# Performance work log

Measured on AMD Instinct MI355X. Metric: run time of the kernel, lower is better.

Reference implementation:

```python
import jax, jax.numpy as jnp
import numpy as np

N_Q = 16
N_K = 16
D_QK = 64
D_V = 64
# torch module default scale=1.0 saturates softmax at feature width 1024;
# we use the conventional sqrt(d) scale for well-conditioned numerics.
SCALE = 32.0  # sqrt(N_Q * D_QK)
DROPOUT_P = 0.0  # dropout is identity at p=0


def setup_inputs() -> dict:
    key = jax.random.key(0)
    kq, kk, kv = jax.random.split(key, 3)
    S = 8192
    return {
        "query": jax.random.normal(kq, (S, N_Q, D_QK), dtype=jnp.float32),
        "key": jax.random.normal(kk, (S, N_K, D_QK), dtype=jnp.float32),
        "value": jax.random.normal(kv, (S, N_K, D_V), dtype=jnp.float32),
    }


def reference(query, key, value):
    # Flatten trailing (head, dim) into one feature axis, as the torch view does.
    q = query.reshape(-1, N_Q * D_QK)            # [S_q, 1024]
    k = key.reshape(-1, N_K * D_QK)              # [S_k, 1024]
    v = value.reshape(-1, N_K * D_V)             # [S_k, 1024]
    scores = jnp.matmul(q, k.T) / SCALE          # [S_q, S_k]
    attn = jax.nn.softmax(scores, axis=-1)       # dropout_p=0 -> identity
    out = jnp.matmul(attn, v)                    # [S_q, 1024]
    return out.reshape(query.shape[:-1] + (-1,))  # [S_q, N_Q, D_V]
```

## Files before the change

kernel.cpp:

```cpp
#include <hip/hip_runtime.h>
#include <hip/hip_bf16.h>


typedef __bf16 bf16x8 __attribute__((ext_vector_type(8)));
typedef float f32x4 __attribute__((ext_vector_type(4)));
typedef const __attribute__((address_space(1))) unsigned int* as1p;
typedef __attribute__((address_space(3))) unsigned int* as3p;
typedef unsigned short u16;

__device__ __forceinline__ u16 f2bf(float x) {
  unsigned u = __float_as_uint(x);
  u += 0x7fffu + ((u >> 16) & 1u);
  return (u16)(u >> 16);
}
__device__ __forceinline__ float bf2f(u16 b) { return __uint_as_float(((unsigned)b) << 16); }
__device__ __forceinline__ unsigned pack2(float lo, float hi) {
  return (unsigned)f2bf(lo) | ((unsigned)f2bf(hi) << 16);
}

#define BAR()   do { __builtin_amdgcn_s_barrier(); asm volatile("" ::: "memory"); } while (0)
#define VM(n)   do { asm volatile("s_waitcnt vmcnt(" #n ")" ::: "memory"); __builtin_amdgcn_sched_barrier(0); } while (0)

__global__ __launch_bounds__(256) void cvt_bf16(const float* __restrict__ in,
                                                unsigned short* __restrict__ out) {
  const size_t i = (size_t)blockIdx.x * 256 + threadIdx.x;
  const float4* p = (const float4*)in + i * 2;
  float4 a = p[0], b = p[1];
  uint4 o;
  o.x = pack2(a.x, a.y);
  o.y = pack2(a.z, a.w);
  o.z = pack2(b.x, b.y);
  o.w = pack2(b.z, b.w);
  ((uint4*)out)[i] = o;
}

__global__ __launch_bounds__(256) void transpose_bf16(const float* __restrict__ V,
                                                      unsigned short* __restrict__ VT) {
  __shared__ float t[64][65];
  const int rb = blockIdx.x * 64;
  const int cb = blockIdx.y * 64;
  const int tid = threadIdx.x;
#pragma unroll
  for (int it = 0; it < 4; ++it) {
    int r = it * 16 + (tid >> 4);
    int c = (tid & 15) * 4;
    float4 x = *(const float4*)(V + (size_t)(rb + r) * 1024 + cb + c);
    t[r][c] = x.x; t[r][c + 1] = x.y; t[r][c + 2] = x.z; t[r][c + 3] = x.w;
  }
  __syncthreads();
  const int j = tid & 63;
  const int c0 = (tid >> 6) * 16;
#pragma unroll
  for (int i = 0; i < 16; ++i) {
    int c = c0 + i;
    VT[(size_t)(cb + c) * 8192 + rb + j] = f2bf(t[j][c]);
  }
}

template <int BM, int DEPTH, int OUTMODE, int DEC>
__global__ __launch_bounds__(512, 2) void gemm_pl(const u16* __restrict__ A,
                                                  const u16* __restrict__ B,
                                                  void* __restrict__ Cv,
                                                  const float* __restrict__ inv,
                                                  float* __restrict__ partials,
                                                  int K, int ldc, float scale) {
  constexpr int MF = BM / 32;
  constexpr int MH = MF / 2;
  constexpr int LAJ = BM / 64;
  constexpr int LPT = LAJ + 4;
  constexpr int ABUF = BM * 128;
  constexpr int BBUF = 32768;
  constexpr int BUFSZ = ABUF + BBUF;
  __shared__ __align__(1024) char smem[DEPTH * BUFSZ];

  const int tid = threadIdx.x;
  const int lane = tid & 63, wave = tid >> 6;
  const int wr = wave >> 2, wc = wave & 3;
  const int lan15 = lane & 15, g = lane >> 4, l7 = lane & 7;

  const int nwg = gridDim.x;
  const int wg = (blockIdx.x & 7) * (nwg >> 3) + (blockIdx.x >> 3);
  int bm0, bn0;
  if constexpr (DEC == 0) {
    const int r = wg & 255;
    bm0 = (r >> 3) * 256;
    bn0 = (((wg >> 8) << 3) | (r & 7)) * 256;
  } else {
    const int chunk = wg >> 5;
    const int within = wg & 31;
    bm0 = (chunk * 8 + (within >> 2)) * BM;
    bn0 = (within & 3) * 256;
  }

  const int sr = tid >> 3;
  const int scb = ((tid & 7) ^ (sr & 7)) * 8;
  const u16* Ags = A + (size_t)(bm0 + sr) * K + scb;
  const u16* Bgs = B + (size_t)(bn0 + sr) * K + scb;

  const int sa0 = ((0 + g) ^ l7) * 16;
  const int sa1 = ((4 + g) ^ l7) * 16;
  const int abase = (wr * (BM / 2) + lan15) * 128;
  const int bbase = ABUF + (wc * 64 + lan15) * 128;

  f32x4 acc[MF][4];
#pragma unroll
  for (int m = 0; m < MF; ++m)
#pragma unroll
    for (int n = 0; n < 4; ++n) acc[m][n] = f32x4{0.f, 0.f, 0.f, 0.f};

  const int nt = K >> 6;

  auto ISSUE = [&](int t) {
    char* bb = smem + (t % DEPTH) * BUFSZ;
    const size_t ko = (size_t)t * 64;
#pragma unroll
    for (int j = 0; j < LAJ; ++j)
      __builtin_amdgcn_global_load_lds((as1p)(Ags + (size_t)j * 64 * K + ko),
                                       (as3p)(bb + j * 8192 + tid * 16), 16, 0, 0);
#pragma unroll
    for (int j = 0; j < 4; ++j)
      __builtin_amdgcn_global_load_lds((as1p)(Bgs + (size_t)j * 64 * K + ko),
                                       (as3p)(bb + ABUF + j * 8192 + tid * 16), 16, 0, 0);
  };

  bf16x8 A0[MH][2], A1[MH][2], B0[2][2], B1[2][2];

  auto RD_A0 = [&](int t) {
    const char* bp = smem + (t % DEPTH) * BUFSZ;
#pragma unroll
    for (int m = 0; m < MH; ++m) {
      A0[m][0] = *(const bf16x8*)(bp + abase + m * 2048 + sa0);
      A0[m][1] = *(const bf16x8*)(bp + abase + m * 2048 + sa1);
    }
  };
  auto RD_A1 = [&](int t) {
    const char* bp = smem + (t % DEPTH) * BUFSZ;
#pragma unroll
    for (int m = 0; m < MH; ++m) {
      A1[m][0] = *(const bf16x8*)(bp + abase + (MH + m) * 2048 + sa0);
      A1[m][1] = *(const bf16x8*)(bp + abase + (MH + m) * 2048 + sa1);
    }
  };
  auto RD_B0 = [&](int t) {
    const char* bp = smem + (t % DEPTH) * BUFSZ;
#pragma unroll
    for (int n = 0; n < 2; ++n) {
      B0[n][0] = *(const bf16x8*)(bp + bbase + n * 2048 + sa0);
      B0[n][1] = *(const bf16x8*)(bp + bbase + n * 2048 + sa1);
    }
  };
  auto RD_B1 = [&](int t) {
    const char* bp = smem + (t % DEPTH) * BUFSZ;
#pragma unroll
    for (int n = 0; n < 2; ++n) {
      B1[n][0] = *(const bf16x8*)(bp + bbase + (2 + n) * 2048 + sa0);
      B1[n][1] = *(const bf16x8*)(bp + bbase + (2 + n) * 2048 + sa1);
    }
  };

  auto Q = [&](bf16x8 (&a)[MH][2], bf16x8 (&b)[2][2], int mo, int no) {
    __builtin_amdgcn_s_setprio(1);
#pragma unroll
    for (int m = 0; m < MH; ++m)
#pragma unroll
      for (int n = 0; n < 2; ++n)
#pragma unroll
        for (int ks = 0; ks < 2; ++ks)
          acc[mo + m][no + n] = __builtin_amdgcn_mfma_f32_16x16x32_bf16(
              a[m][ks], b[n][ks], acc[mo + m][no + n], 0, 0, 0);
    __builtin_amdgcn_s_setprio(0);
  };

  ISSUE(0);
  if constexpr (DEPTH == 3) {
    ISSUE(1);
    if constexpr (LPT == 8) { VM(8); } else { VM(6); }
  } else {
    VM(0);
  }
  BAR();
  RD_A0(0); RD_B0(0);

  for (int t = 0; t < nt; ++t) {
    BAR();
    if constexpr (DEPTH == 2) {
      if (t + 1 < nt) ISSUE(t + 1);
    } else {
      if (t + 2 < nt) ISSUE(t + 2);
    }
    RD_B1(t);
    Q(A0, B0, 0, 0);
    RD_A1(t);
    Q(A0, B1, 0, 2);
    if constexpr (DEPTH == 2) {
      if (t + 1 < nt) { VM(0); }
    } else {
      if (t + 2 < nt) {
        if constexpr (LPT == 8) { VM(8); } else { VM(6); }
      } else if (t + 1 < nt) {
        VM(0);
      }
    }
    Q(A1, B0, MH, 0);
    if (t + 1 < nt) { RD_A0(t + 1); RD_B0(t + 1); }
    Q(A1, B1, MH, 2);
  }

  const int c0 = bn0 + wc * 64 + lan15;
  if constexpr (OUTMODE == 0) {
    u16* C = (u16*)Cv;
    const int cb4 = (bn0 >> 8) * 4 + wc;
#pragma unroll
    for (int m = 0; m < MF; ++m)
#pragma unroll
      for (int r = 0; r < 4; ++r) {
        const int row = bm0 + wr * (BM / 2) + m * 16 + g * 4 + r;
        float part = 0.f;
#pragma unroll
        for (int n = 0; n < 4; ++n) {
          float v = __expf(acc[m][n][r] * scale);
          C[(size_t)row * ldc + c0 + n * 16] = f2bf(v);
          part += v;
        }
        part += __shfl_xor(part, 1, 64);
        part += __shfl_xor(part, 2, 64);
        part += __shfl_xor(part, 4, 64);
        part += __shfl_xor(part, 8, 64);
        if (lan15 == 0) partials[(size_t)row * 128 + cb4] = part;
      }
  } else {
    float* C = (float*)Cv;
#pragma unroll
    for (int m = 0; m < MF; ++m)
#pragma unroll
      for (int r = 0; r < 4; ++r) {
        const int row = bm0 + wr * (BM / 2) + m * 16 + g * 4 + r;
        const float iv = inv ? inv[row] : 1.0f;
#pragma unroll
        for (int n = 0; n < 4; ++n)
          C[(size_t)row * ldc + c0 + n * 16] = acc[m][n][r] * iv;
      }
  }
}

__global__ __launch_bounds__(256) void rowinv(const float* __restrict__ partials,
                                              float* __restrict__ inv) {
  const int row = blockIdx.x * 256 + threadIdx.x;
  const float4* p = (const float4*)(partials + (size_t)row * 128);
  float s = 0.f;
#pragma unroll
  for (int j = 0; j < 32; ++j) {
    float4 v = p[j];
    s += (v.x + v.y) + (v.z + v.w);
  }
  inv[row] = 1.0f / s;
}

__global__ __launch_bounds__(256) void normalize_inplace(u16* __restrict__ E) {
  __shared__ float red[4];
  u16* row = E + (size_t)blockIdx.x * 8192;
  const int tid = threadIdx.x;
  float f[32];
  float s = 0.f;
#pragma unroll
  for (int c = 0; c < 4; ++c) {
    uint4 v = *((const uint4*)row + c * 256 + tid);
    unsigned u[4] = {v.x, v.y, v.z, v.w};
#pragma unroll
    for (int q = 0; q < 4; ++q) {
      f[c * 8 + q * 2] = bf2f((u16)(u[q] & 0xffffu));
      f[c * 8 + q * 2 + 1] = bf2f((u16)(u[q] >> 16));
      s += f[c * 8 + q * 2] + f[c * 8 + q * 2 + 1];
    }
  }
#pragma unroll
  for (int off = 32; off; off >>= 1) s += __shfl_xor(s, off, 64);
  if ((tid & 63) == 0) red[tid >> 6] = s;
  __syncthreads();
  const float iv = 1.0f / ((red[0] + red[1]) + (red[2] + red[3]));
#pragma unroll
  for (int c = 0; c < 4; ++c) {
    uint4 o;
    o.x = pack2(f[c * 8 + 0] * iv, f[c * 8 + 1] * iv);
    o.y = pack2(f[c * 8 + 2] * iv, f[c * 8 + 3] * iv);
    o.z = pack2(f[c * 8 + 4] * iv, f[c * 8 + 5] * iv);
    o.w = pack2(f[c * 8 + 6] * iv, f[c * 8 + 7] * iv);
    *((uint4*)row + c * 256 + tid) = o;
  }
}

extern "C" void kernel_launch(void* const* d_in, const int* in_sizes, int n_in,
                              void* d_out, int out_size, void* d_ws, size_t ws_size,
                              hipStream_t stream) {
  const float* Q = (const float*)d_in[0];
  const float* K = (const float*)d_in[1];
  const float* V = (const float*)d_in[2];

  char* ws = (char*)d_ws;
  u16* S = (u16*)ws;
  u16* VT = (u16*)(ws + (size_t)134217728);
  float* partials = (float*)(ws + (size_t)134217728 + 16777216);
  float* inv = (float*)(ws + (size_t)134217728 + 16777216 + 4194304);
  const bool haveInv =
      ws_size >= (size_t)134217728 + 16777216 + 4194304 + 32768;

  u16* Qb = (u16*)d_out;
  u16* Kb = Qb + 8388608;

  cvt_bf16<<<4096, 256, 0, stream>>>(Q, Qb);
  cvt_bf16<<<4096, 256, 0, stream>>>(K, Kb);
  transpose_bf16<<<dim3(128, 16), 256, 0, stream>>>(V, VT);

  gemm_pl<256, 2, 0, 0><<<1024, 512, 0, stream>>>(
      Qb, Kb, S, nullptr, haveInv ? partials : (float*)(ws + 134217728 + 16777216),
      1024, 8192, 1.0f / 32.0f);

  if (haveInv) {
    rowinv<<<32, 256, 0, stream>>>(partials, inv);
    gemm_pl<128, 3, 1, 1><<<256, 512, 0, stream>>>(
        S, VT, d_out, inv, nullptr, 8192, 1024, 1.0f);
  } else {
    normalize_inplace<<<8192, 256, 0, stream>>>(S);
    gemm_pl<128, 3, 1, 1><<<256, 512, 0, stream>>>(
        S, VT, d_out, nullptr, nullptr, 8192, 1024, 1.0f);
  }
}
```

Before: 307.3 us.

## Replace PV GEMM with double-buffered 8-wave kernel interleaving loads and MFMA phases

Adds a new GEMM kernel (gemm8d) with two LDS buffers. Global-to-LDS loads for the next k-tiles are split into quarter chunks and interleaved between four MFMA phases. Barriers and explicit waitcnts order the phases, and s_setprio raises priority around the MFMA blocks. The attention-times-V GEMM now uses this kernel so that memory latency hides behind matrix math better than in the previous 3-stage pipeline. The cost is many more barriers per iteration and reliance on hand-placed wait counts, which could break if the compiler reorders memory operations.

```diff
diff --git a/kernel.cpp b/kernel.cpp
--- a/kernel.cpp
+++ b/kernel.cpp
@@ -20,6 +20,9 @@
 
 #define BAR()   do { __builtin_amdgcn_s_barrier(); asm volatile("" ::: "memory"); } while (0)
 #define VM(n)   do { asm volatile("s_waitcnt vmcnt(" #n ")" ::: "memory"); __builtin_amdgcn_sched_barrier(0); } while (0)
+#define BARX()   __builtin_amdgcn_s_barrier()
+#define WAITL()  asm volatile("s_waitcnt lgkmcnt(0)")
+#define WAITV(n) asm volatile("s_waitcnt vmcnt(" #n ")")
 
 __global__ __launch_bounds__(256) void cvt_bf16(const float* __restrict__ in,
                                                 unsigned short* __restrict__ out) {
@@ -243,6 +246,192 @@
   }
 }
 
+template <int BM, int OUTMODE, int DEC>
+__global__ __launch_bounds__(512, 2) void gemm8d(const u16* __restrict__ A,
+                                                 const u16* __restrict__ B,
+                                                 void* __restrict__ Cv,
+                                                 const float* __restrict__ inv,
+                                                 float* __restrict__ partials,
+                                                 int K, int ldc, float scale) {
+  constexpr int MF = BM / 32;
+  constexpr int MH = MF / 2;
+  constexpr int ABUF = BM * 128;
+  constexpr int BBUF = 32768;
+  constexpr int BUFSZ = ABUF + BBUF;
+  __shared__ __align__(1024) char smem[2 * BUFSZ];
+
+  const int tid = threadIdx.x;
+  const int lane = tid & 63, wave = tid >> 6;
+  const int wr = wave >> 2, wc = wave & 3;
+  const int lan15 = lane & 15, g = lane >> 4, l7 = lane & 7;
+
+  const int nwg = gridDim.x;
+  const int wg = (blockIdx.x & 7) * (nwg >> 3) + (blockIdx.x >> 3);
+  int bm0, bn0;
+  if constexpr (DEC == 0) {
+    const int r = wg & 255;
+    bm0 = (r >> 3) * 256;
+    bn0 = (((wg >> 8) << 3) | (r & 7)) * 256;
+  } else {
+    const int chunk = wg >> 5;
+    const int within = wg & 31;
+    bm0 = (chunk * 8 + (within >> 2)) * BM;
+    bn0 = (within & 3) * 256;
+  }
+
+  const int sr = tid >> 3;
+  const int scb = ((tid & 7) ^ (sr & 7)) * 8;
+  const u16* Ags = A + (size_t)(bm0 + sr) * K + scb;
+  const u16* Bgs = B + (size_t)(bn0 + sr) * K + scb;
+
+  const int sa0 = ((0 + g) ^ l7) * 16;
+  const int sa1 = ((4 + g) ^ l7) * 16;
+  const int abase = (wr * (BM / 2) + lan15) * 128;
+  const int bbase = ABUF + (wc * 64 + lan15) * 128;
+
+  f32x4 acc[MF][4];
+#pragma unroll
+  for (int m = 0; m < MF; ++m)
+#pragma unroll
+    for (int n = 0; n < 4; ++n) acc[m][n] = f32x4{0.f, 0.f, 0.f, 0.f};
+
+  const int nt = K >> 6;
+  const int niter = nt >> 1;
+
+  auto IA = [&](int t, int ja, int jb) {
+    char* bb = smem + (t & 1) * BUFSZ;
+    const size_t ko = (size_t)t * 64;
+    __builtin_amdgcn_global_load_lds((as1p)(Ags + (size_t)ja * 64 * K + ko),
+                                     (as3p)(bb + ja * 8192 + tid * 16), 16, 0, 0);
+    __builtin_amdgcn_global_load_lds((as1p)(Ags + (size_t)jb * 64 * K + ko),
+                                     (as3p)(bb + jb * 8192 + tid * 16), 16, 0, 0);
+  };
+  auto IB = [&](int t, int j0) {
+    char* bb = smem + (t & 1) * BUFSZ + ABUF;
+    const size_t ko = (size_t)t * 64;
+    __builtin_amdgcn_global_load_lds((as1p)(Bgs + (size_t)j0 * 64 * K + ko),
+                                     (as3p)(bb + j0 * 8192 + tid * 16), 16, 0, 0);
+    __builtin_amdgcn_global_load_lds((as1p)(Bgs + (size_t)(j0 + 1) * 64 * K + ko),
+                                     (as3p)(bb + (j0 + 1) * 8192 + tid * 16), 16, 0, 0);
+  };
+  auto IA_mh0 = [&](int t) { if constexpr (BM == 256) IA(t, 0, 2); };
+  auto IA_mh1 = [&](int t) { if constexpr (BM == 256) IA(t, 1, 3); else IA(t, 0, 1); };
+
+  bf16x8 a[MH][2], b[4][2];
+  auto DS_A = [&](int bb, int mh) {
+#pragma unroll
+    for (int m = 0; m < MH; ++m) {
+      a[m][0] = *(const bf16x8*)(smem + bb + abase + (mh * MH + m) * 2048 + sa0);
+      a[m][1] = *(const bf16x8*)(smem + bb + abase + (mh * MH + m) * 2048 + sa1);
+    }
+  };
+  auto DS_B = [&](int bb, int nh) {
+#pragma unroll
+    for (int n = 0; n < 2; ++n) {
+      b[nh * 2 + n][0] = *(const bf16x8*)(smem + bb + bbase + (nh * 2 + n) * 2048 + sa0);
+      b[nh * 2 + n][1] = *(const bf16x8*)(smem + bb + bbase + (nh * 2 + n) * 2048 + sa1);
+    }
+  };
+  auto MMA = [&](int mh, int nh) {
+    __builtin_amdgcn_s_setprio(1);
+#pragma unroll
+    for (int m = 0; m < MH; ++m)
+#pragma unroll
+      for (int n = 0; n < 2; ++n)
+#pragma unroll
+        for (int ks = 0; ks < 2; ++ks)
+          acc[mh * MH + m][nh * 2 + n] = __builtin_amdgcn_mfma_f32_16x16x32_bf16(
+              a[m][ks], b[nh * 2 + n][ks], acc[mh * MH + m][nh * 2 + n], 0, 0, 0);
+    __builtin_amdgcn_s_setprio(0);
+  };
+
+  if constexpr (BM == 256) {
+    IA(0, 0, 2); IB(0, 0); IB(0, 2); IA(0, 1, 3);
+    IA(1, 0, 2); IB(1, 0); IB(1, 2);
+    WAITV(6);
+  } else {
+    IB(0, 0); IB(0, 2); IA(0, 0, 1);
+    IB(1, 0); IB(1, 2);
+    WAITV(4);
+  }
+  BARX();
+
+  for (int i = 0; i < niter; ++i) {
+    const int t0 = 2 * i;
+    const bool more = (i + 1 < niter);
+
+    DS_A(0, 0); DS_B(0, 0);
+    IA_mh1(t0 + 1);
+    BARX(); WAITL(); MMA(0, 0); BARX();
+
+    DS_B(0, 1);
+    if (more) IA_mh0(t0 + 2);
+    BARX(); WAITL(); MMA(0, 1); BARX();
+
+    DS_A(0, 1);
+    if (more) IB(t0 + 2, 0);
+    BARX(); WAITL(); MMA(1, 0); BARX();
+
+    if (more) IB(t0 + 2, 2);
+    BARX(); MMA(1, 1);
+    if (more) { if constexpr (BM == 256) WAITV(6); else WAITV(4); } else { WAITV(0); }
+    BARX();
+
+    DS_A(BUFSZ, 0); DS_B(BUFSZ, 0);
+    if (more) IA_mh1(t0 + 2);
+    BARX(); WAITL(); MMA(0, 0); BARX();
+
+    DS_B(BUFSZ, 1);
+    if (more) IA_mh0(t0 + 3);
+    BARX(); WAITL(); MMA(0, 1); BARX();
+
+    DS_A(BUFSZ, 1);
+    if (more) IB(t0 + 3, 0);
+    BARX(); WAITL(); MMA(1, 0); BARX();
+
+    if (more) IB(t0 + 3, 2);
+    BARX(); MMA(1, 1);
+    if (more) { if constexpr (BM == 256) WAITV(6); else WAITV(4); } else { WAITV(0); }
+    BARX();
+  }
+
+  const int c0 = bn0 + wc * 64 + lan15;
+  if constexpr (OUTMODE == 0) {
+    u16* C = (u16*)Cv;
+    const int cb4 = (bn0 >> 8) * 4 + wc;
+#pragma unroll
+    for (int m = 0; m < MF; ++m)
+#pragma unroll
+      for (int r = 0; r < 4; ++r) {
+        const int row = bm0 + wr * (BM / 2) + m * 16 + g * 4 + r;
+        float part = 0.f;
+#pragma unroll
+        for (int n = 0; n < 4; ++n) {
+          float v = __expf(acc[m][n][r] * scale);
+          C[(size_t)row * ldc + c0 + n * 16] = f2bf(v);
+          part += v;
+        }
+        part += __shfl_xor(part, 1, 64);
+        part += __shfl_xor(part, 2, 64);
+        part += __shfl_xor(part, 4, 64);
+        part += __shfl_xor(part, 8, 64);
+        if (lan15 == 0) partials[(size_t)row * 128 + cb4] = part;
+      }
+  } else {
+    float* C = (float*)Cv;
+#pragma unroll
+    for (int m = 0; m < MF; ++m)
+#pragma unroll
+      for (int r = 0; r < 4; ++r) {
+        const int row = bm0 + wr * (BM / 2) + m * 16 + g * 4 + r;
+        const float iv = inv ? inv[row] : 1.0f;
+#pragma unroll
+        for (int n = 0; n < 4; ++n)
+          C[(size_t)row * ldc + c0 + n * 16] = acc[m][n][r] * iv;
+      }
+  }
+}
+
 __global__ __launch_bounds__(256) void rowinv(const float* __restrict__ partials,
                                               float* __restrict__ inv) {
   const int row = blockIdx.x * 256 + threadIdx.x;
@@ -317,11 +506,11 @@
 
   if (haveInv) {
     rowinv<<<32, 256, 0, stream>>>(partials, inv);
-    gemm_pl<128, 3, 1, 1><<<256, 512, 0, stream>>>(
+    gemm8d<128, 1, 1><<<256, 512, 0, stream>>>(
         S, VT, d_out, inv, nullptr, 8192, 1024, 1.0f);
   } else {
     normalize_inplace<<<8192, 256, 0, stream>>>(S);
-    gemm_pl<128, 3, 1, 1><<<256, 512, 0, stream>>>(
+    gemm8d<128, 1, 1><<<256, 512, 0, stream>>>(
         S, VT, d_out, nullptr, nullptr, 8192, 1024, 1.0f);
   }
 }
```

Measured after the change: 303.7 us. Within noise of the previous version (-1.2%).
